# Kernel tuning notes

Measured on AMD Instinct MI355X. Metric: run time of the kernel, lower is better.

Reference implementation:

```python
import jax, jax.numpy as jnp
import numpy as np

B, F, H, D, K = 16384, 4096, 512, 64, 512  # batch, feat, hidden, emb_dim, codebook size
M = H // D  # code positions per sample


def _leaky(h):
    return jnp.where(h > 0, h, 0.01 * h)


def setup_inputs() -> dict:
    key = jax.random.key(0)
    ks = jax.random.split(key, 16)
    lin = lambda k, i, o: jax.random.normal(k, (i, o), jnp.float32) * (1.0 / np.sqrt(i))
    return {
        "x": jax.random.uniform(ks[0], (B, F), jnp.float32),
        "We1": lin(ks[1], F, 256), "be1": jnp.zeros((256,), jnp.float32),
        "We2": lin(ks[2], 256, 128), "be2": jnp.zeros((128,), jnp.float32),
        "We3": lin(ks[3], 128, H), "be3": jnp.zeros((H,), jnp.float32),
        "Wd1": lin(ks[4], H, 128), "bd1": jnp.zeros((128,), jnp.float32),
        "Wd2": lin(ks[5], 128, 256), "bd2": jnp.zeros((256,), jnp.float32),
        "Wd3": lin(ks[6], 256, F), "bd3": jnp.zeros((F,), jnp.float32),
        "codebook": jax.random.normal(ks[7], (D, K), jnp.float32) * 0.02,  # (emb_dim, num_embeddings)
    }


def _nearest(z_e, codebook):
    # z_e: (B, D, M); codebook: (D, K). Squared-distance argmin over K.
    x2 = jnp.sum(z_e * z_e, axis=1)                       # (B, M)
    xw = jnp.einsum('bdm,dk->bmk', z_e, codebook)         # (B, M, K)
    w2 = jnp.sum(codebook * codebook, axis=0)             # (K,)
    idx = jnp.argmin(x2[..., None] - 2.0 * xw + w2, axis=-1)  # (B, M)
    quant = jnp.swapaxes(codebook.T[idx], 1, 2)           # (B, D, M)
    return quant, idx


def reference(x, We1, be1, We2, be2, We3, be3, Wd1, bd1, Wd2, bd2, Wd3, bd3, codebook):
    # encoder MLP
    h = _leaky(x @ We1 + be1)
    h = _leaky(h @ We2 + be2)
    h = _leaky(h @ We3 + be3)                             # (B, H)
    z_e = h.reshape(B, D, M)
    # emb(z_e, weight_sg=True): straight-through, weight detached
    quant_sg, idx = _nearest(z_e, jax.lax.stop_gradient(codebook))
    z_q = z_e + jax.lax.stop_gradient(quant_sg - z_e)
    # emb(z_e.detach()): grads (if any) flow to codebook via gather
    emb, _ = _nearest(jax.lax.stop_gradient(z_e), codebook)
    # decoder MLP
    g = _leaky(z_q.reshape(B, H) @ Wd1 + bd1)
    g = _leaky(g @ Wd2 + bd2)
    X_pred = jax.nn.sigmoid(g @ Wd3 + bd3)                # (B, F)
    return idx, z_e, z_q, emb, X_pred
```

## Files before the change

### kernel.cpp

```cpp
#include <hip/hip_runtime.h>
#include <cstdint>
#include <cstddef>


static constexpr int BB = 16384;

typedef __attribute__((ext_vector_type(8))) short short8;
typedef __attribute__((ext_vector_type(8))) _Float16 half8;
typedef __attribute__((ext_vector_type(4))) float f32x4;

__device__ __forceinline__ unsigned short f2bf(float f) {
    union { float f; uint32_t u; } v; v.f = f;
    uint32_t r = (v.u + 0x7FFFu + ((v.u >> 16) & 1u)) >> 16;
    return (unsigned short)r;
}

#define GLL16(gp, lp) \
    __builtin_amdgcn_global_load_lds( \
        (const __attribute__((address_space(1))) uint32_t*)(gp), \
        (__attribute__((address_space(3))) uint32_t*)(lp), 16, 0, 0)

__global__ __launch_bounds__(256) void combine_act(
    const float* __restrict__ part, int S, size_t MN,
    const float* __restrict__ bias, int N,
    float* __restrict__ outF, unsigned short* __restrict__ outB)
{
    const size_t e = ((size_t)blockIdx.x * 256 + threadIdx.x) * 4;
    if (e >= MN) return;
    float4 s = *(const float4*)(part + e);
    for (int i = 1; i < S; i++) {
        const float4 p = *(const float4*)(part + (size_t)i * MN + e);
        s.x += p.x; s.y += p.y; s.z += p.z; s.w += p.w;
    }
    const int col = (int)(e & (size_t)(N - 1));
    const float4 bv = *(const float4*)(bias + col);
    float v0 = s.x + bv.x, v1 = s.y + bv.y, v2 = s.z + bv.z, v3 = s.w + bv.w;
    v0 = (v0 > 0.f) ? v0 : 0.01f * v0;
    v1 = (v1 > 0.f) ? v1 : 0.01f * v1;
    v2 = (v2 > 0.f) ? v2 : 0.01f * v2;
    v3 = (v3 > 0.f) ? v3 : 0.01f * v3;
    if (outF) {
        float4 o; o.x = v0; o.y = v1; o.z = v2; o.w = v3;
        *(float4*)(outF + e) = o;
    } else {
        ushort4 o; o.x = f2bf(v0); o.y = f2bf(v1); o.z = f2bf(v2); o.w = f2bf(v3);
        *(ushort4*)(outB + e) = o;
    }
}

__global__ __launch_bounds__(256) void transpose_cast(
    const float* __restrict__ W, unsigned short* __restrict__ WT, int R, int Cc)
{
    __shared__ float s[32][33];
    const int tx = threadIdx.x & 31, ty = threadIdx.x >> 5;
    const int c0 = blockIdx.x * 32, r0 = blockIdx.y * 32;
#pragma unroll
    for (int i = 0; i < 4; i++)
        s[ty + i * 8][tx] = W[(size_t)(r0 + ty + i * 8) * Cc + c0 + tx];
    __syncthreads();
#pragma unroll
    for (int i = 0; i < 4; i++)
        WT[(size_t)(c0 + ty + i * 8) * R + r0 + tx] = f2bf(s[tx][ty + i * 8]);
}

__global__ __launch_bounds__(256) void transpose_split_f16(
    const float* __restrict__ W, unsigned short* __restrict__ Th,
    unsigned short* __restrict__ Tl, int R, int Cc)
{
    __shared__ float s[32][33];
    const int tx = threadIdx.x & 31, ty = threadIdx.x >> 5;
    const int c0 = blockIdx.x * 32, r0 = blockIdx.y * 32;
#pragma unroll
    for (int i = 0; i < 4; i++)
        s[ty + i * 8][tx] = W[(size_t)(r0 + ty + i * 8) * Cc + c0 + tx];
    __syncthreads();
#pragma unroll
    for (int i = 0; i < 4; i++) {
        const float f = s[tx][ty + i * 8];
        const _Float16 h = (_Float16)f;
        const float fh = (float)h;
        const _Float16 lo = (_Float16)((f - fh) * 4096.0f);
        union { _Float16 hf; unsigned short u; } ch, cl;
        ch.hf = h; cl.hf = lo;
        Th[(size_t)(c0 + ty + i * 8) * R + r0 + tx] = ch.u;
        Tl[(size_t)(c0 + ty + i * 8) * R + r0 + tx] = cl.u;
    }
}

template<int BUF>
__device__ __forceinline__ void enc1_step(
    int K0,
    const float* __restrict__ gA,
    const unsigned short* __restrict__ gBh,
    const unsigned short* __restrict__ gBl,
    short (&Ah)[2][2048], short (&Al)[2][2048],
    half8 (&bhC)[4], half8 (&bhN)[4], half8 (&blS)[4],
    f32x4& p0, f32x4& p1,
    f32x4 (&acc1)[4][4], f32x4 (&acc2)[4][4],
    int aoff, int fr0)
{
    constexpr size_t rstep = (size_t)16 * 4096;
    const int kn1 = K0 + 32, kn2 = K0 + 64;
    __syncthreads();
#pragma unroll
    for (int j = 0; j < 4; j++)
        blS[j] = *(const half8*)(gBl + (size_t)j * rstep + K0);
    if (kn1 < 2048) {
#pragma unroll
        for (int j = 0; j < 4; j++)
            bhN[j] = *(const half8*)(gBh + (size_t)j * rstep + kn1);
    }
    f32x4 f0, f1;
    if (kn2 < 2048) {
        f0 = __builtin_nontemporal_load((const f32x4*)(gA + kn2));
        f1 = __builtin_nontemporal_load((const f32x4*)(gA + kn2 + 4));
    }
    half8 ah[4];
#pragma unroll
    for (int i = 0; i < 4; i++)
        ah[i] = *(const half8*)&Ah[BUF][(i << 9) + fr0];
#pragma unroll
    for (int i = 0; i < 4; i++)
#pragma unroll
        for (int j = 0; j < 4; j++)
            acc1[i][j] = __builtin_amdgcn_mfma_f32_16x16x32_f16(
                ah[i], bhC[j], acc1[i][j], 0, 0, 0);
#pragma unroll
    for (int i = 0; i < 4; i++)
#pragma unroll
        for (int j = 0; j < 4; j++)
            acc2[i][j] = __builtin_amdgcn_mfma_f32_16x16x32_f16(
                ah[i], blS[j], acc2[i][j], 0, 0, 0);
    half8 al[4];
#pragma unroll
    for (int i = 0; i < 4; i++)
        al[i] = *(const half8*)&Al[BUF][(i << 9) + fr0];
#pragma unroll
    for (int i = 0; i < 4; i++)
#pragma unroll
        for (int j = 0; j < 4; j++)
            acc2[i][j] = __builtin_amdgcn_mfma_f32_16x16x32_f16(
                al[i], bhC[j], acc2[i][j], 0, 0, 0);
    if (kn1 < 2048) {
        float fv[8];
        *(f32x4*)&fv[0] = p0;
        *(f32x4*)&fv[4] = p1;
        union { _Float16 h[8]; short8 s; } uh, ul;
#pragma unroll
        for (int e = 0; e < 8; e++) {
            const float f = fv[e];
            const _Float16 h = (_Float16)f;
            const float fh = (float)h;
            uh.h[e] = h;
            ul.h[e] = (_Float16)((f - fh) * 4096.0f);
        }
        *(short8*)&Ah[BUF ^ 1][aoff] = uh.s;
        *(short8*)&Al[BUF ^ 1][aoff] = ul.s;
    }
    if (kn2 < 2048) { p0 = f0; p1 = f1; }
}

__global__ __launch_bounds__(256, 2) void gemm_f16x2_enc1(
    const float* __restrict__ X,
    const unsigned short* __restrict__ Bh,
    const unsigned short* __restrict__ Bl,
    float* __restrict__ part)
{
    __shared__ short Ah[2][2048];
    __shared__ short Al[2][2048];
    const int tid = threadIdx.x;
    const int l = tid & 63, w = tid >> 6;
    const int lm = l & 15, lq = l >> 4;
    const int bm = blockIdx.y * 64;
    const int kStart = blockIdx.z * 2048;

    const float* gA = X + (size_t)(bm + w * 16 + lm) * 4096 + kStart + lq * 8;
    const unsigned short* gBh = Bh + (size_t)(w * 64 + lm) * 4096 + kStart + lq * 8;
    const unsigned short* gBl = Bl + (size_t)(w * 64 + lm) * 4096 + kStart + lq * 8;
    constexpr size_t rstep = (size_t)16 * 4096;

    const int aoff = (w << 9) + (l << 3);
    const int fr0 = (lq << 7) + (lm << 3);

    f32x4 acc1[4][4], acc2[4][4];
#pragma unroll
    for (int i = 0; i < 4; i++)
#pragma unroll
        for (int j = 0; j < 4; j++) {
            acc1[i][j] = (f32x4){0.f, 0.f, 0.f, 0.f};
            acc2[i][j] = (f32x4){0.f, 0.f, 0.f, 0.f};
        }

    half8 bhA[4], bhB[4], blS[4];
    f32x4 p0, p1;

    {
#pragma unroll
        for (int j = 0; j < 4; j++)
            bhA[j] = *(const half8*)(gBh + (size_t)j * rstep);
        f32x4 a0 = __builtin_nontemporal_load((const f32x4*)(gA));
        f32x4 a1 = __builtin_nontemporal_load((const f32x4*)(gA + 4));
        p0 = __builtin_nontemporal_load((const f32x4*)(gA + 32));
        p1 = __builtin_nontemporal_load((const f32x4*)(gA + 36));
        float fv[8];
        *(f32x4*)&fv[0] = a0;
        *(f32x4*)&fv[4] = a1;
        union { _Float16 h[8]; short8 s; } uh, ul;
#pragma unroll
        for (int e = 0; e < 8; e++) {
            const float f = fv[e];
            const _Float16 h = (_Float16)f;
            const float fh = (float)h;
            uh.h[e] = h;
            ul.h[e] = (_Float16)((f - fh) * 4096.0f);
        }
        *(short8*)&Ah[0][aoff] = uh.s;
        *(short8*)&Al[0][aoff] = ul.s;
    }

    for (int k2 = 0; k2 < 2048; k2 += 64) {
        enc1_step<0>(k2,      gA, gBh, gBl, Ah, Al, bhA, bhB, blS,
                     p0, p1, acc1, acc2, aoff, fr0);
        enc1_step<1>(k2 + 32, gA, gBh, gBl, Ah, Al, bhB, bhA, blS,
                     p0, p1, acc1, acc2, aoff, fr0);
    }

    float* P = part + (size_t)blockIdx.z * BB * 256;
    const float inv = 0.000244140625f;
#pragma unroll
    for (int i = 0; i < 4; i++)
#pragma unroll
        for (int j = 0; j < 4; j++) {
            const int col = w * 64 + j * 16 + lm;
#pragma unroll
            for (int r = 0; r < 4; r++) {
                const int row = bm + i * 16 + lq * 4 + r;
                P[(size_t)row * 256 + col] = acc1[i][j][r] + inv * acc2[i][j][r];
            }
        }
}

template<int BUF, int NJ, int KLEN>
__device__ __forceinline__ void mid_step(
    int K0,
    const float* __restrict__ gA,
    const unsigned short* __restrict__ gBh,
    const unsigned short* __restrict__ gBl,
    short (&Ah)[2][2048], short (&Al)[2][2048],
    half8 (&bhC)[NJ], half8 (&bhN)[NJ], half8 (&blS)[NJ],
    f32x4& p0, f32x4& p1,
    f32x4 (&acc1)[4][NJ], f32x4 (&acc2)[4][NJ],
    int aoff, int fr0)
{
    constexpr size_t rstep = (size_t)16 * KLEN;
    const int kn1 = K0 + 32, kn2 = K0 + 64;
    __syncthreads();
#pragma unroll
    for (int j = 0; j < NJ; j++)
        blS[j] = *(const half8*)(gBl + (size_t)j * rstep + K0);
    if (kn1 < KLEN) {
#pragma unroll
        for (int j = 0; j < NJ; j++)
            bhN[j] = *(const half8*)(gBh + (size_t)j * rstep + kn1);
    }
    f32x4 f0, f1;
    if (kn2 < KLEN) {
        f0 = *(const f32x4*)(gA + kn2);
        f1 = *(const f32x4*)(gA + kn2 + 4);
    }
    half8 ah[4];
#pragma unroll
    for (int i = 0; i < 4; i++)
        ah[i] = *(const half8*)&Ah[BUF][(i << 9) + fr0];
#pragma unroll
    for (int i = 0; i < 4; i++)
#pragma unroll
        for (int j = 0; j < NJ; j++)
            acc1[i][j] = __builtin_amdgcn_mfma_f32_16x16x32_f16(
                ah[i], bhC[j], acc1[i][j], 0, 0, 0);
#pragma unroll
    for (int i = 0; i < 4; i++)
#pragma unroll
        for (int j = 0; j < NJ; j++)
            acc2[i][j] = __builtin_amdgcn_mfma_f32_16x16x32_f16(
                ah[i], blS[j], acc2[i][j], 0, 0, 0);
    half8 al[4];
#pragma unroll
    for (int i = 0; i < 4; i++)
        al[i] = *(const half8*)&Al[BUF][(i << 9) + fr0];
#pragma unroll
    for (int i = 0; i < 4; i++)
#pragma unroll
        for (int j = 0; j < NJ; j++)
            acc2[i][j] = __builtin_amdgcn_mfma_f32_16x16x32_f16(
                al[i], bhC[j], acc2[i][j], 0, 0, 0);
    if (kn1 < KLEN) {
        float fv[8];
        *(f32x4*)&fv[0] = p0;
        *(f32x4*)&fv[4] = p1;
        union { _Float16 h[8]; short8 s; } uh, ul;
#pragma unroll
        for (int e = 0; e < 8; e++) {
            const float f = fv[e];
            const _Float16 h = (_Float16)f;
            const float fh = (float)h;
            uh.h[e] = h;
            ul.h[e] = (_Float16)((f - fh) * 4096.0f);
        }
        *(short8*)&Ah[BUF ^ 1][aoff] = uh.s;
        *(short8*)&Al[BUF ^ 1][aoff] = ul.s;
    }
    if (kn2 < KLEN) { p0 = f0; p1 = f1; }
}

template<int NJ, int KLEN, int ACT>
__global__ __launch_bounds__(256, 2) void gemm_f16x2_mid(
    const float* __restrict__ A,
    const unsigned short* __restrict__ Bh,
    const unsigned short* __restrict__ Bl,
    const float* __restrict__ bias,
    float* __restrict__ Cf, unsigned short* __restrict__ Cb)
{
    __shared__ short Ah[2][2048];
    __shared__ short Al[2][2048];
    const int tid = threadIdx.x;
    const int l = tid & 63, w = tid >> 6;
    const int lm = l & 15, lq = l >> 4;
    const int bm = blockIdx.y * 64;
    const int bn = blockIdx.x * (64 * NJ);
    const int N = gridDim.x * 64 * NJ;

    const float* gA = A + (size_t)(bm + w * 16 + lm) * KLEN + lq * 8;
    const unsigned short* gBh = Bh + (size_t)(bn + w * (16 * NJ) + lm) * KLEN + lq * 8;
    const unsigned short* gBl = Bl + (size_t)(bn + w * (16 * NJ) + lm) * KLEN + lq * 8;
    constexpr size_t rstep = (size_t)16 * KLEN;

    const int aoff = (w << 9) + (l << 3);
    const int fr0 = (lq << 7) + (lm << 3);

    f32x4 acc1[4][NJ], acc2[4][NJ];
#pragma unroll
    for (int i = 0; i < 4; i++)
#pragma unroll
        for (int j = 0; j < NJ; j++) {
            acc1[i][j] = (f32x4){0.f, 0.f, 0.f, 0.f};
            acc2[i][j] = (f32x4){0.f, 0.f, 0.f, 0.f};
        }

    half8 bhA[NJ], bhB[NJ], blS[NJ];
    f32x4 p0, p1;

    {
#pragma unroll
        for (int j = 0; j < NJ; j++)
            bhA[j] = *(const half8*)(gBh + (size_t)j * rstep);
        f32x4 a0 = *(const f32x4*)(gA);
        f32x4 a1 = *(const f32x4*)(gA + 4);
        p0 = *(const f32x4*)(gA + 32);
        p1 = *(const f32x4*)(gA + 36);
        float fv[8];
        *(f32x4*)&fv[0] = a0;
        *(f32x4*)&fv[4] = a1;
        union { _Float16 h[8]; short8 s; } uh, ul;
#pragma unroll
        for (int e = 0; e < 8; e++) {
            const float f = fv[e];
            const _Float16 h = (_Float16)f;
            const float fh = (float)h;
            uh.h[e] = h;
            ul.h[e] = (_Float16)((f - fh) * 4096.0f);
        }
        *(short8*)&Ah[0][aoff] = uh.s;
        *(short8*)&Al[0][aoff] = ul.s;
    }

    for (int k2 = 0; k2 < KLEN; k2 += 64) {
        mid_step<0, NJ, KLEN>(k2,      gA, gBh, gBl, Ah, Al, bhA, bhB, blS,
                              p0, p1, acc1, acc2, aoff, fr0);
        mid_step<1, NJ, KLEN>(k2 + 32, gA, gBh, gBl, Ah, Al, bhB, bhA, blS,
                              p0, p1, acc1, acc2, aoff, fr0);
    }

    const float inv = 0.000244140625f;
#pragma unroll
    for (int i = 0; i < 4; i++)
#pragma unroll
        for (int j = 0; j < NJ; j++) {
            const int col = bn + w * (16 * NJ) + j * 16 + lm;
            const float bv = bias[col];
#pragma unroll
            for (int r = 0; r < 4; r++) {
                const int row = bm + i * 16 + lq * 4 + r;
                float v = acc1[i][j][r] + inv * acc2[i][j][r] + bv;
                v = (v > 0.f) ? v : 0.01f * v;
                if (ACT == 0) Cf[(size_t)row * N + col] = v;
                else          Cb[(size_t)row * N + col] = f2bf(v);
            }
        }
}

__global__ __launch_bounds__(256) void gemm_bf16_dec3(
    const unsigned short* __restrict__ Ag,
    const unsigned short* __restrict__ Bt,
    const float* __restrict__ bias, float* __restrict__ C)
{
    __shared__ short As[4096];
    __shared__ short Bs2[4096];
    const int tid = threadIdx.x;
    const int l = tid & 63, w = tid >> 6;
    const int lm = l & 15, lq = l >> 4;
    const int bm = blockIdx.y * 128, bn = blockIdx.x * 128;
    const int wm = (w >> 1) * 64, wn = (w & 1) * 64;

    const int t0 = w * 2, t1 = w * 2 + 1;
    const unsigned short* ga0 = Ag + (size_t)(bm + t0 * 16 + lm) * 256 + lq * 8;
    const unsigned short* ga1 = Ag + (size_t)(bm + t1 * 16 + lm) * 256 + lq * 8;
    const unsigned short* gb0 = Bt + (size_t)(bn + t0 * 16 + lm) * 256 + lq * 8;
    const unsigned short* gb1 = Bt + (size_t)(bn + t1 * 16 + lm) * 256 + lq * 8;

    f32x4 acc[4][4];
#pragma unroll
    for (int i = 0; i < 4; i++)
#pragma unroll
        for (int j = 0; j < 4; j++) acc[i][j] = (f32x4){0.f, 0.f, 0.f, 0.f};

    for (int k0 = 0; k0 < 256; k0 += 32) {
        __syncthreads();
        GLL16(ga0 + k0, &As[t0 * 512]);
        GLL16(ga1 + k0, &As[t1 * 512]);
        GLL16(gb0 + k0, &Bs2[t0 * 512]);
        GLL16(gb1 + k0, &Bs2[t1 * 512]);
        __syncthreads();
        short8 af[4], bf[4];
#pragma unroll
        for (int i = 0; i < 4; i++)
            af[i] = *(const short8*)&As[((w >> 1) * 4 + i) * 512 + lq * 128 + lm * 8];
#pragma unroll
        for (int j = 0; j < 4; j++)
            bf[j] = *(const short8*)&Bs2[((w & 1) * 4 + j) * 512 + lq * 128 + lm * 8];
#pragma unroll
        for (int i = 0; i < 4; i++)
#pragma unroll
            for (int j = 0; j < 4; j++)
                acc[i][j] = __builtin_amdgcn_mfma_f32_16x16x32_bf16(
                    af[i], bf[j], acc[i][j], 0, 0, 0);
    }

#pragma unroll
    for (int i = 0; i < 4; i++) {
#pragma unroll
        for (int j = 0; j < 4; j++) {
            const int col = bn + wn + j * 16 + lm;
            const float bv = bias[col];
#pragma unroll
            for (int r = 0; r < 4; r++) {
                const int row = bm + wm + i * 16 + lq * 4 + r;
                float v = acc[i][j][r] + bv;
                v = 1.0f / (1.0f + __expf(-v));
                C[(size_t)row * 4096 + col] = v;
            }
        }
    }
}

__global__ __launch_bounds__(512) void vq_argmin(
    const float* __restrict__ ze, const float* __restrict__ cb,
    float* __restrict__ idxf)
{
    __shared__ float cbs[64 * 512];
    __shared__ float As[64][68];
    __shared__ float w2s[512];
    const int tid = threadIdx.x;
    const int p0 = blockIdx.x * 64;

    const float4* cb4 = (const float4*)cb;
    float4* cbs4 = (float4*)cbs;
    for (int i = tid; i < 8192; i += 512) cbs4[i] = cb4[i];

    const float4* ze4 = (const float4*)(ze + (size_t)p0 * 64);
    for (int i = tid; i < 1024; i += 512) {
        float4 v = ze4[i];
        int e = i * 4;
        int bo = e >> 9, r = e & 511;
        int d = r >> 3, m = r & 7;
        *(float4*)&As[d][bo * 8 + m] = v;
    }
    __syncthreads();

    {
        float s = 0.f;
#pragma unroll
        for (int d = 0; d < 64; ++d) { float c = cbs[d * 512 + tid]; s = fmaf(c, c, s); }
        w2s[tid] = s;
    }
    __syncthreads();

    const int tx = tid & 63;
    const int ty = tid >> 6;

    float acc[8][8], x2a[8];
#pragma unroll
    for (int i = 0; i < 8; i++) {
        x2a[i] = 0.f;
#pragma unroll
        for (int j = 0; j < 8; j++) acc[i][j] = 0.f;
    }

#pragma unroll 8
    for (int kk = 0; kk < 64; ++kk) {
        float a[8], b[8];
        *(float4*)&a[0] = *(const float4*)&As[kk][ty * 8];
        *(float4*)&a[4] = *(const float4*)&As[kk][ty * 8 + 4];
        *(float4*)&b[0] = *(const float4*)&cbs[kk * 512 + tx * 8];
        *(float4*)&b[4] = *(const float4*)&cbs[kk * 512 + tx * 8 + 4];
#pragma unroll
        for (int i = 0; i < 8; i++) x2a[i] = fmaf(a[i], a[i], x2a[i]);
#pragma unroll
        for (int i = 0; i < 8; i++)
#pragma unroll
            for (int j = 0; j < 8; j++)
                acc[i][j] = fmaf(a[i], b[j], acc[i][j]);
    }

    float w2v[8];
#pragma unroll
    for (int j = 0; j < 8; j++) w2v[j] = w2s[tx * 8 + j];

#pragma unroll
    for (int i = 0; i < 8; i++) {
        float bd = 3.4e38f; int bk = 1 << 30;
#pragma unroll
        for (int j = 0; j < 8; j++) {
            float dsc = (x2a[i] - 2.0f * acc[i][j]) + w2v[j];
            if (dsc < bd) { bd = dsc; bk = tx * 8 + j; }
        }
        for (int off = 32; off > 0; off >>= 1) {
            float od = __shfl_xor(bd, off);
            int   ok = __shfl_xor(bk, off);
            if (od < bd || (od == bd && ok < bk)) { bd = od; bk = ok; }
        }
        if (tx == i) idxf[p0 + ty * 8 + i] = (float)bk;
    }
}

__global__ __launch_bounds__(256) void vq_gather(
    const float* __restrict__ ze, const float* __restrict__ idxf,
    const float* __restrict__ cb,
    float* __restrict__ zq, float* __restrict__ emb)
{
    const int t = blockIdx.x * 256 + threadIdx.x;
    const int e = t * 4;
    const int b = e >> 9, r = e & 511;
    const int d = r >> 3, m = r & 7;
    const float4 z = *(const float4*)(ze + e);
    float q[4];
#pragma unroll
    for (int c = 0; c < 4; c++) {
        int k = (int)idxf[b * 8 + m + c];
        q[c] = cb[d * 512 + k];
    }
    float4 zq4, em4;
    zq4.x = z.x + (q[0] - z.x); zq4.y = z.y + (q[1] - z.y);
    zq4.z = z.z + (q[2] - z.z); zq4.w = z.w + (q[3] - z.w);
    em4.x = q[0]; em4.y = q[1]; em4.z = q[2]; em4.w = q[3];
    *(float4*)(zq + e) = zq4;
    *(float4*)(emb + e) = em4;
}

extern "C" void kernel_launch(void* const* d_in, const int* in_sizes, int n_in,
                              void* d_out, int out_size, void* d_ws, size_t ws_size,
                              hipStream_t stream)
{
    const float* x   = (const float*)d_in[0];
    const float* We1 = (const float*)d_in[1];
    const float* be1 = (const float*)d_in[2];
    const float* We2 = (const float*)d_in[3];
    const float* be2 = (const float*)d_in[4];
    const float* We3 = (const float*)d_in[5];
    const float* be3 = (const float*)d_in[6];
    const float* Wd1 = (const float*)d_in[7];
    const float* bd1 = (const float*)d_in[8];
    const float* Wd2 = (const float*)d_in[9];
    const float* bd2 = (const float*)d_in[10];
    const float* Wd3 = (const float*)d_in[11];
    const float* bd3 = (const float*)d_in[12];
    const float* cb  = (const float*)d_in[13];

    float* out   = (float*)d_out;
    float* o_idx = out;
    float* o_ze  = o_idx + 131072;
    float* o_zq  = o_ze + 8388608;
    float* o_emb = o_zq + 8388608;
    float* o_X   = o_emb + 8388608;

    float* h1 = (float*)d_ws;
    float* h2 = h1 + (size_t)BB * 256;
    float* g1 = h1;
    unsigned short* g2b = (unsigned short*)(h1 + (size_t)BB * 128);
    unsigned short* WT  = (unsigned short*)h2;

    unsigned short* Bth  = (unsigned short*)(o_X + 16777216);
    unsigned short* Btl  = Bth + 1048576;
    unsigned short* W2h  = Btl + 1048576;
    unsigned short* W2l  = W2h + 32768;
    unsigned short* W3h  = W2l + 32768;
    unsigned short* W3l  = W3h + 65536;
    unsigned short* Wd1h = W3l + 65536;
    unsigned short* Wd1l = Wd1h + 65536;
    unsigned short* Wd2h = Wd1l + 65536;
    unsigned short* Wd2l = Wd2h + 32768;

    transpose_split_f16<<<dim3(8, 128), 256, 0, stream>>>(We1, Bth, Btl, 4096, 256);
    transpose_split_f16<<<dim3(4, 8),   256, 0, stream>>>(We2, W2h, W2l, 256, 128);
    transpose_split_f16<<<dim3(16, 4),  256, 0, stream>>>(We3, W3h, W3l, 128, 512);
    transpose_split_f16<<<dim3(4, 16),  256, 0, stream>>>(Wd1, Wd1h, Wd1l, 512, 128);
    transpose_split_f16<<<dim3(8, 4),   256, 0, stream>>>(Wd2, Wd2h, Wd2l, 128, 256);

    gemm_f16x2_enc1<<<dim3(1, 256, 2), 256, 0, stream>>>(x, Bth, Btl, o_X);
    combine_act<<<4096, 256, 0, stream>>>(o_X, 2, (size_t)BB * 256, be1, 256, h1, nullptr);
    gemm_f16x2_mid<2, 256, 0><<<dim3(1, 256), 256, 0, stream>>>(
        h1, W2h, W2l, be2, h2, nullptr);
    gemm_f16x2_mid<4, 128, 0><<<dim3(2, 256), 256, 0, stream>>>(
        h2, W3h, W3l, be3, o_ze, nullptr);

    vq_argmin<<<dim3(2048), dim3(512), 0, stream>>>(o_ze, cb, o_idx);
    vq_gather<<<dim3(8192), dim3(256), 0, stream>>>(o_ze, o_idx, cb, o_zq, o_emb);

    transpose_cast<<<dim3(128, 8), 256, 0, stream>>>(Wd3, WT, 256, 4096);

    gemm_f16x2_mid<2, 512, 0><<<dim3(1, 256), 256, 0, stream>>>(
        o_zq, Wd1h, Wd1l, bd1, g1, nullptr);
    gemm_f16x2_mid<4, 128, 1><<<dim3(1, 256), 256, 0, stream>>>(
        g1, Wd2h, Wd2l, bd2, nullptr, g2b);
    gemm_bf16_dec3<<<dim3(32, 128), 256, 0, stream>>>(g2b, WT, bd3, o_X);
}
```

Before: 980.1 us.

## Fuse VQ gather into argmin, drop LDS staging in dec3 GEMM, tighten barriers

Result: slower. 1.033 ms (+5.4%).

```diff
diff --git a/kernel.cpp b/kernel.cpp
--- a/kernel.cpp
+++ b/kernel.cpp
@@ -15,15 +15,16 @@
     return (unsigned short)r;
 }
 
-#define GLL16(gp, lp) \
-    __builtin_amdgcn_global_load_lds( \
-        (const __attribute__((address_space(1))) uint32_t*)(gp), \
-        (__attribute__((address_space(3))) uint32_t*)(lp), 16, 0, 0)
+__device__ __forceinline__ void lds_barrier() {
+    asm volatile("s_waitcnt lgkmcnt(0)" ::: "memory");
+    __builtin_amdgcn_s_barrier();
+    __builtin_amdgcn_sched_barrier(0);
+}
 
 __global__ __launch_bounds__(256) void combine_act(
     const float* __restrict__ part, int S, size_t MN,
     const float* __restrict__ bias, int N,
-    float* __restrict__ outF, unsigned short* __restrict__ outB)
+    float* __restrict__ outF)
 {
     const size_t e = ((size_t)blockIdx.x * 256 + threadIdx.x) * 4;
     if (e >= MN) return;
@@ -39,13 +40,8 @@
     v1 = (v1 > 0.f) ? v1 : 0.01f * v1;
     v2 = (v2 > 0.f) ? v2 : 0.01f * v2;
     v3 = (v3 > 0.f) ? v3 : 0.01f * v3;
-    if (outF) {
-        float4 o; o.x = v0; o.y = v1; o.z = v2; o.w = v3;
-        *(float4*)(outF + e) = o;
-    } else {
-        ushort4 o; o.x = f2bf(v0); o.y = f2bf(v1); o.z = f2bf(v2); o.w = f2bf(v3);
-        *(ushort4*)(outB + e) = o;
-    }
+    float4 o; o.x = v0; o.y = v1; o.z = v2; o.w = v3;
+    *(float4*)(outF + e) = o;
 }
 
 __global__ __launch_bounds__(256) void transpose_cast(
@@ -101,7 +97,7 @@
 {
     constexpr size_t rstep = (size_t)16 * 4096;
     const int kn1 = K0 + 32, kn2 = K0 + 64;
-    __syncthreads();
+    lds_barrier();
 #pragma unroll
     for (int j = 0; j < 4; j++)
         blS[j] = *(const half8*)(gBl + (size_t)j * rstep + K0);
@@ -254,7 +250,7 @@
 {
     constexpr size_t rstep = (size_t)16 * KLEN;
     const int kn1 = K0 + 32, kn2 = K0 + 64;
-    __syncthreads();
+    lds_barrier();
 #pragma unroll
     for (int j = 0; j < NJ; j++)
         blS[j] = *(const half8*)(gBl + (size_t)j * rstep + K0);
@@ -399,24 +395,43 @@
         }
 }
 
+__device__ __forceinline__ void dec3_step(
+    int kn,
+    const unsigned short* __restrict__ gA,
+    const unsigned short* __restrict__ gB,
+    short8 (&afC)[4], short8 (&bfC)[4],
+    short8 (&afN)[4], short8 (&bfN)[4],
+    f32x4 (&acc)[4][4])
+{
+    if (kn < 256) {
+#pragma unroll
+        for (int i = 0; i < 4; i++)
+            afN[i] = *(const short8*)(gA + (size_t)i * 16 * 256 + kn);
+#pragma unroll
+        for (int j = 0; j < 4; j++)
+            bfN[j] = *(const short8*)(gB + (size_t)j * 16 * 256 + kn);
+    }
+#pragma unroll
+    for (int i = 0; i < 4; i++)
+#pragma unroll
+        for (int j = 0; j < 4; j++)
+            acc[i][j] = __builtin_amdgcn_mfma_f32_16x16x32_bf16(
+                afC[i], bfC[j], acc[i][j], 0, 0, 0);
+}
+
 __global__ __launch_bounds__(256) void gemm_bf16_dec3(
     const unsigned short* __restrict__ Ag,
     const unsigned short* __restrict__ Bt,
     const float* __restrict__ bias, float* __restrict__ C)
 {
-    __shared__ short As[4096];
-    __shared__ short Bs2[4096];
     const int tid = threadIdx.x;
     const int l = tid & 63, w = tid >> 6;
     const int lm = l & 15, lq = l >> 4;
     const int bm = blockIdx.y * 128, bn = blockIdx.x * 128;
     const int wm = (w >> 1) * 64, wn = (w & 1) * 64;
 
-    const int t0 = w * 2, t1 = w * 2 + 1;
-    const unsigned short* ga0 = Ag + (size_t)(bm + t0 * 16 + lm) * 256 + lq * 8;
-    const unsigned short* ga1 = Ag + (size_t)(bm + t1 * 16 + lm) * 256 + lq * 8;
-    const unsigned short* gb0 = Bt + (size_t)(bn + t0 * 16 + lm) * 256 + lq * 8;
-    const unsigned short* gb1 = Bt + (size_t)(bn + t1 * 16 + lm) * 256 + lq * 8;
+    const unsigned short* gA = Ag + (size_t)(bm + wm + lm) * 256 + lq * 8;
+    const unsigned short* gB = Bt + (size_t)(bn + wn + lm) * 256 + lq * 8;
 
     f32x4 acc[4][4];
 #pragma unroll
@@ -424,26 +439,17 @@
 #pragma unroll
         for (int j = 0; j < 4; j++) acc[i][j] = (f32x4){0.f, 0.f, 0.f, 0.f};
 
-    for (int k0 = 0; k0 < 256; k0 += 32) {
-        __syncthreads();
-        GLL16(ga0 + k0, &As[t0 * 512]);
-        GLL16(ga1 + k0, &As[t1 * 512]);
-        GLL16(gb0 + k0, &Bs2[t0 * 512]);
-        GLL16(gb1 + k0, &Bs2[t1 * 512]);
-        __syncthreads();
-        short8 af[4], bf[4];
-#pragma unroll
-        for (int i = 0; i < 4; i++)
-            af[i] = *(const short8*)&As[((w >> 1) * 4 + i) * 512 + lq * 128 + lm * 8];
-#pragma unroll
-        for (int j = 0; j < 4; j++)
-            bf[j] = *(const short8*)&Bs2[((w & 1) * 4 + j) * 512 + lq * 128 + lm * 8];
-#pragma unroll
-        for (int i = 0; i < 4; i++)
-#pragma unroll
-            for (int j = 0; j < 4; j++)
-                acc[i][j] = __builtin_amdgcn_mfma_f32_16x16x32_bf16(
-                    af[i], bf[j], acc[i][j], 0, 0, 0);
+    short8 afA[4], afB[4], bfA[4], bfB[4];
+#pragma unroll
+    for (int i = 0; i < 4; i++)
+        afA[i] = *(const short8*)(gA + (size_t)i * 16 * 256);
+#pragma unroll
+    for (int j = 0; j < 4; j++)
+        bfA[j] = *(const short8*)(gB + (size_t)j * 16 * 256);
+
+    for (int k0 = 0; k0 < 256; k0 += 64) {
+        dec3_step(k0 + 32, gA, gB, afA, bfA, afB, bfB, acc);
+        dec3_step(k0 + 64, gA, gB, afB, bfB, afA, bfA, acc);
     }
 
 #pragma unroll
@@ -465,17 +471,19 @@
 
 __global__ __launch_bounds__(512) void vq_argmin(
     const float* __restrict__ ze, const float* __restrict__ cb,
-    float* __restrict__ idxf)
-{
-    __shared__ float cbs[64 * 512];
+    float* __restrict__ idxf, float* __restrict__ zq, float* __restrict__ emb)
+{
+    __shared__ float cbs[64 * 516];
     __shared__ float As[64][68];
     __shared__ float w2s[512];
+    __shared__ int ids[64];
     const int tid = threadIdx.x;
     const int p0 = blockIdx.x * 64;
 
     const float4* cb4 = (const float4*)cb;
     float4* cbs4 = (float4*)cbs;
-    for (int i = tid; i < 8192; i += 512) cbs4[i] = cb4[i];
+    for (int i = tid; i < 8192; i += 512)
+        cbs4[(i >> 7) * 129 + (i & 127)] = cb4[i];
 
     const float4* ze4 = (const float4*)(ze + (size_t)p0 * 64);
     for (int i = tid; i < 1024; i += 512) {
@@ -490,7 +498,7 @@
     {
         float s = 0.f;
 #pragma unroll
-        for (int d = 0; d < 64; ++d) { float c = cbs[d * 512 + tid]; s = fmaf(c, c, s); }
+        for (int d = 0; d < 64; ++d) { float c = cbs[d * 516 + tid]; s = fmaf(c, c, s); }
         w2s[tid] = s;
     }
     __syncthreads();
@@ -511,8 +519,8 @@
         float a[8], b[8];
         *(float4*)&a[0] = *(const float4*)&As[kk][ty * 8];
         *(float4*)&a[4] = *(const float4*)&As[kk][ty * 8 + 4];
-        *(float4*)&b[0] = *(const float4*)&cbs[kk * 512 + tx * 8];
-        *(float4*)&b[4] = *(const float4*)&cbs[kk * 512 + tx * 8 + 4];
+#pragma unroll
+        for (int j = 0; j < 8; j++) b[j] = cbs[kk * 516 + tx + j * 64];
 #pragma unroll
         for (int i = 0; i < 8; i++) x2a[i] = fmaf(a[i], a[i], x2a[i]);
 #pragma unroll
@@ -524,7 +532,7 @@
 
     float w2v[8];
 #pragma unroll
-    for (int j = 0; j < 8; j++) w2v[j] = w2s[tx * 8 + j];
+    for (int j = 0; j < 8; j++) w2v[j] = w2s[tx + j * 64];
 
 #pragma unroll
     for (int i = 0; i < 8; i++) {
@@ -532,39 +540,38 @@
 #pragma unroll
         for (int j = 0; j < 8; j++) {
             float dsc = (x2a[i] - 2.0f * acc[i][j]) + w2v[j];
-            if (dsc < bd) { bd = dsc; bk = tx * 8 + j; }
+            int kc = tx + j * 64;
+            if (dsc < bd || (dsc == bd && kc < bk)) { bd = dsc; bk = kc; }
         }
         for (int off = 32; off > 0; off >>= 1) {
             float od = __shfl_xor(bd, off);
             int   ok = __shfl_xor(bk, off);
             if (od < bd || (od == bd && ok < bk)) { bd = od; bk = ok; }
         }
-        if (tx == i) idxf[p0 + ty * 8 + i] = (float)bk;
-    }
-}
-
-__global__ __launch_bounds__(256) void vq_gather(
-    const float* __restrict__ ze, const float* __restrict__ idxf,
-    const float* __restrict__ cb,
-    float* __restrict__ zq, float* __restrict__ emb)
-{
-    const int t = blockIdx.x * 256 + threadIdx.x;
-    const int e = t * 4;
-    const int b = e >> 9, r = e & 511;
-    const int d = r >> 3, m = r & 7;
-    const float4 z = *(const float4*)(ze + e);
-    float q[4];
-#pragma unroll
-    for (int c = 0; c < 4; c++) {
-        int k = (int)idxf[b * 8 + m + c];
-        q[c] = cb[d * 512 + k];
-    }
-    float4 zq4, em4;
-    zq4.x = z.x + (q[0] - z.x); zq4.y = z.y + (q[1] - z.y);
-    zq4.z = z.z + (q[2] - z.z); zq4.w = z.w + (q[3] - z.w);
-    em4.x = q[0]; em4.y = q[1]; em4.z = q[2]; em4.w = q[3];
-    *(float4*)(zq + e) = zq4;
-    *(float4*)(emb + e) = em4;
+        if (tx == i) {
+            idxf[p0 + ty * 8 + i] = (float)bk;
+            ids[ty * 8 + i] = bk;
+        }
+    }
+
+    __syncthreads();
+    const int bl_ = tid >> 6, dd = tid & 63;
+    const int kbase = bl_ * 8;
+    float zq8[8], em8[8];
+#pragma unroll
+    for (int mm = 0; mm < 8; mm++) {
+        const int k = ids[kbase + mm];
+        const float q = cbs[dd * 516 + k];
+        const float z = As[dd][kbase + mm];
+        em8[mm] = q;
+        zq8[mm] = z + (q - z);
+    }
+    float* zqp = zq + (size_t)p0 * 64 + bl_ * 512 + dd * 8;
+    float* emp = emb + (size_t)p0 * 64 + bl_ * 512 + dd * 8;
+    *(float4*)zqp = *(float4*)&zq8[0];
+    *(float4*)(zqp + 4) = *(float4*)&zq8[4];
+    *(float4*)emp = *(float4*)&em8[0];
+    *(float4*)(emp + 4) = *(float4*)&em8[4];
 }
 
 extern "C" void kernel_launch(void* const* d_in, const int* in_sizes, int n_in,
@@ -617,16 +624,15 @@
     transpose_split_f16<<<dim3(8, 4),   256, 0, stream>>>(Wd2, Wd2h, Wd2l, 128, 256);
 
     gemm_f16x2_enc1<<<dim3(1, 256, 2), 256, 0, stream>>>(x, Bth, Btl, o_X);
-    combine_act<<<4096, 256, 0, stream>>>(o_X, 2, (size_t)BB * 256, be1, 256, h1, nullptr);
+    combine_act<<<4096, 256, 0, stream>>>(o_X, 2, (size_t)BB * 256, be1, 256, h1);
     gemm_f16x2_mid<2, 256, 0><<<dim3(1, 256), 256, 0, stream>>>(
         h1, W2h, W2l, be2, h2, nullptr);
     gemm_f16x2_mid<4, 128, 0><<<dim3(2, 256), 256, 0, stream>>>(
         h2, W3h, W3l, be3, o_ze, nullptr);
 
-    vq_argmin<<<dim3(2048), dim3(512), 0, stream>>>(o_ze, cb, o_idx);
-    vq_gather<<<dim3(8192), dim3(256), 0, stream>>>(o_ze, o_idx, cb, o_zq, o_emb);
-
     transpose_cast<<<dim3(128, 8), 256, 0, stream>>>(Wd3, WT, 256, 4096);
+
+    vq_argmin<<<dim3(2048), dim3(512), 0, stream>>>(o_ze, cb, o_idx, o_zq, o_emb);
 
     gemm_f16x2_mid<2, 512, 0><<<dim3(1, 256), 256, 0, stream>>>(
         o_zq, Wd1h, Wd1l, bd1, g1, nullptr);
```
